# Kernel tuning notes

Hardware: AMD Instinct MI355X
Metric: run time of the kernel (lower is better)

Reference implementation:

```python
import jax, jax.numpy as jnp
import numpy as np
import math

B, T, N, FIN, C, E = 32, 10, 1000, 1, 96, 8000
NEG_SLOPE = 0.2


def _sinusoidal_pos_embed(stepsize, embedding_size):
    position = jnp.arange(stepsize, dtype=jnp.float32)[:, None]
    div_term = jnp.exp(jnp.arange(0, embedding_size, 2, dtype=jnp.float32)
                       * (-math.log(10000.0) / embedding_size))
    pe = jnp.zeros((stepsize, embedding_size), dtype=jnp.float32)
    pe = pe.at[:, 0::2].set(jnp.sin(position * div_term))
    pe = pe.at[:, 1::2].set(jnp.cos(position * div_term))
    return pe  # [T, C]


def setup_inputs() -> dict:
    key = jax.random.key(0)
    k_x, k_s, k_d, k_wl, k_wr, k_a = jax.random.split(key, 6)
    x = jax.random.normal(k_x, (B, T, N, FIN), dtype=jnp.float32)
    src = jax.random.randint(k_s, (E,), 0, N)
    dst = jax.random.randint(k_d, (E,), 0, N)
    edge_index = jnp.stack([src, dst]).astype(jnp.int32)
    s_in = 1.0 / np.sqrt(FIN)
    Wl = jax.random.uniform(k_wl, (FIN, C), jnp.float32, -s_in, s_in)
    Wr = jax.random.uniform(k_wr, (FIN, C), jnp.float32, -s_in, s_in)
    bl = jnp.zeros((C,), jnp.float32)
    br = jnp.zeros((C,), jnp.float32)
    s_a = 1.0 / np.sqrt(C)
    att = jax.random.uniform(k_a, (C,), jnp.float32, -s_a, s_a)
    bias = jnp.zeros((C,), jnp.float32)
    return dict(x=x, edge_index=edge_index, Wl=Wl, bl=bl, Wr=Wr, br=br,
                att=att, bias=bias)


def reference(x, edge_index, Wl, bl, Wr, br, att, bias):
    Bb, Tt, Nn, Fin = x.shape
    Cc = Wl.shape[1]
    # GATv2Conv default add_self_loops=True
    loops = jnp.arange(Nn, dtype=edge_index.dtype)
    src = jnp.concatenate([edge_index[0], loops])  # message sources j
    dst = jnp.concatenate([edge_index[1], loops])  # message targets i

    xg = x.reshape(Bb * Tt, Nn, Fin)                 # [G, N, Fin]
    xl = xg @ Wl + bl                                # lin_l(x_j)  [G, N, C]
    xr = xg @ Wr + br                                # lin_r(x_i)  [G, N, C]

    # GATv2 attention logits: a^T LeakyReLU(xl[j] + xr[i])
    e = jax.nn.leaky_relu(xl[:, src] + xr[:, dst], NEG_SLOPE) @ att  # [G, Etot]

    def per_graph(e_g, xl_g):
        m = jax.ops.segment_max(e_g, dst, num_segments=Nn)
        ex = jnp.exp(e_g - m[dst])
        denom = jax.ops.segment_sum(ex, dst, num_segments=Nn)
        alpha = ex / denom[dst]                       # softmax over incoming edges
        msgs = alpha[:, None] * xl_g[src]             # [Etot, C]
        return jax.ops.segment_sum(msgs, dst, num_segments=Nn)  # [N, C]

    out = jax.vmap(per_graph)(e, xl) + bias           # [G, N, C]
    out = out.reshape(Bb, Tt, Nn, Cc)

    pos = _sinusoidal_pos_embed(Tt, Cc)               # [T, C]
    out = out + pos[None, :, None, :]
    return out.reshape(Bb, Tt * Nn, Cc)
```

## Files before the change

kernel.cpp:

```cpp
#include <hip/hip_runtime.h>
#include <math.h>

#define G_ 320
#define N_ 1000
#define T_ 10
#define C_ 96
#define E_ 8000
#define QN 250
#define CAP 2816
#define NTB 129

__global__ __launch_bounds__(256, 6) void kAll(
        const float* __restrict__ x, const int* __restrict__ ei,
        const float* __restrict__ Wl, const float* __restrict__ bl,
        const float* __restrict__ Wr, const float* __restrict__ br,
        const float* __restrict__ att, const float* __restrict__ bias,
        float4* __restrict__ out) {
    __shared__ float xgs[N_];
    __shared__ int   slots[CAP];
    __shared__ int   cnt[256], cur[256], offsL[260];
    __shared__ float tabL[2 * NTB];
    __shared__ float Sloc[QN];
    __shared__ float4 wl4[C_ / 4], cb4[C_ / 4];
    __shared__ float lin4[4];

    const int tid = threadIdx.x;
    const int q = blockIdx.x, g = blockIdx.y;
    const int lo = q * QN;
    const int t = g % T_;

    if (tid < N_ / 4)
        ((float4*)xgs)[tid] = ((const float4*)(x + (size_t)g * N_))[tid];
    cnt[tid] = (tid < QN) ? 1 : 0;
    if (tid < C_) {
        int k2 = tid & ~1;
        float dt = __expf(-(float)k2 * (logf(10000.0f) / (float)C_));
        float ang = (float)t * dt;
        float pe = (tid & 1) ? cosf(ang) : sinf(ang);
        ((float*)wl4)[tid] = Wl[tid];
        ((float*)cb4)[tid] = bl[tid] + bias[tid] + pe;
    }
    {
        int w = tid >> 6, lane = tid & 63;
        if (w < 3) {
            float s = 0.f;
            for (int i = lane; i < C_; i += 64) {
                float a = att[i];
                float m = (w == 0) ? Wl[i] : (w == 1) ? Wr[i] : (bl[i] + br[i]);
                s += a * m;
            }
            for (int off = 32; off; off >>= 1) s += __shfl_down(s, off);
            if (lane == 0) lin4[w] = 0.6f * s;
        } else {
            float m = 0.f;
            for (int i = lane; i < C_; i += 64) m = fmaxf(m, fabsf(bl[i] + br[i]));
            for (int off = 32; off; off >>= 1) m = fmaxf(m, __shfl_down(m, off));
            if (lane == 0) lin4[3] = (m == 0.f) ? 1.f : 0.f;
        }
    }
    for (int i = tid; i < 2 * NTB; i += 256) {
        int which = (i >= NTB);
        int j = i - which * NTB;
        float tt = -1.f + (float)j * (2.f / (float)(NTB - 1));
        float s = 0.f;
        for (int c = 0; c < C_; c++) {
            float wl = Wl[c], wr = Wr[c];
            float val = which ? fmaf(tt, wl, wr) : fmaf(tt, wr, wl);
            s = fmaf(0.4f * att[c], fabsf(val), s);
        }
        tabL[i] = s;
    }
    __syncthreads();

    const int4* d4 = (const int4*)(ei + E_);
    const int4* s4 = (const int4*)ei;
    for (int j = tid; j < E_ / 4; j += 256) {
        int4 d = d4[j];
        int r0 = d.x - lo, r1 = d.y - lo, r2 = d.z - lo, r3 = d.w - lo;
        if ((unsigned)r0 < (unsigned)QN) atomicAdd(&cnt[r0], 1);
        if ((unsigned)r1 < (unsigned)QN) atomicAdd(&cnt[r1], 1);
        if ((unsigned)r2 < (unsigned)QN) atomicAdd(&cnt[r2], 1);
        if ((unsigned)r3 < (unsigned)QN) atomicAdd(&cnt[r3], 1);
    }
    __syncthreads();

    if (tid < 64) {
        int b4 = tid * 4;
        int a0 = cnt[b4], a1 = cnt[b4 + 1], a2 = cnt[b4 + 2], a3 = cnt[b4 + 3];
        int s1 = a0 + a1, s2 = s1 + a2, s3 = s2 + a3;
        int pre = s3;
        for (int off = 1; off < 64; off <<= 1) {
            int tv = __shfl_up(pre, off);
            if (tid >= off) pre += tv;
        }
        int base = pre - s3;
        offsL[b4] = base;          cur[b4] = base;
        offsL[b4 + 1] = base + a0; cur[b4 + 1] = base + a0;
        offsL[b4 + 2] = base + s1; cur[b4 + 2] = base + s1;
        offsL[b4 + 3] = base + s2; cur[b4 + 3] = base + s2;
    }
    __syncthreads();

    for (int j = tid; j < E_ / 4; j += 256) {
        int4 d = d4[j];
        int4 s = s4[j];
#define SCAT(DD, SS) { int r = (DD) - lo;                                    \
        if ((unsigned)r < (unsigned)QN) {                                    \
            int pos = atomicAdd(&cur[r], 1);                                 \
            slots[pos] = (SS) | ((DD) << 16); } }
        SCAT(d.x, s.x) SCAT(d.y, s.y) SCAT(d.z, s.z) SCAT(d.w, s.w)
#undef SCAT
    }
    if (tid < QN) {
        int nid = lo + tid;
        int pos = atomicAdd(&cur[tid], 1);
        slots[pos] = nid | (nid << 16);
    }
    __syncthreads();

    const float la = lin4[0], lb = lin4[1], lc = lin4[2];
    const bool homog = (lin4[3] != 0.f);
    if (tid < QN) {
        int a = offsL[tid], b = offsL[tid + 1];
        float m = -INFINITY, den = 0.f, num = 0.f;
        if (homog) {
            for (int p = a; p < b; ++p) {
                int sd = slots[p];
                float uu = xgs[sd & 0xFFFF], vv = xgs[sd >> 16];
                float au = fabsf(uu), av = fabsf(vv);
                bool ub = au >= av;
                float big = ub ? au : av;
                float tt = (ub ? vv : uu) / (ub ? uu : vv);
                tt = fmaxf(fminf(tt, 1.f), -1.f);
                float fi = fmaf(tt, 64.f, 64.f);
                int i0 = (int)fi; i0 = min(i0, NTB - 2);
                float fr = fi - (float)i0;
                int bse = ub ? 0 : NTB;
                float t0 = tabL[bse + i0], t1 = tabL[bse + i0 + 1];
                float l = fmaf(big, fmaf(fr, t1 - t0, t0),
                               fmaf(uu, la, fmaf(vv, lb, lc)));
                float nm = fmaxf(m, l);
                float sc = __expf(m - nm);
                float ex = __expf(l - nm);
                den = den * sc + ex;
                num = fmaf(ex, uu, num * sc);
                m = nm;
            }
        } else {
            for (int p = a; p < b; ++p) {
                int sd = slots[p];
                float uu = xgs[sd & 0xFFFF], vv = xgs[sd >> 16];
                float a2 = 0.f;
                for (int c = 0; c < C_; c++) {
                    float wv = fmaf(uu, Wl[c], fmaf(vv, Wr[c], bl[c] + br[c]));
                    a2 = fmaf(0.4f * att[c], fabsf(wv), a2);
                }
                float l = fmaf(uu, la, fmaf(vv, lb, lc)) + a2;
                float nm = fmaxf(m, l);
                float sc = __expf(m - nm);
                float ex = __expf(l - nm);
                den = den * sc + ex;
                num = fmaf(ex, uu, num * sc);
                m = nm;
            }
        }
        Sloc[tid] = num / den;
    }
    __syncthreads();

    float4* out4 = out + (size_t)(g * N_ + lo) * (C_ / 4);
    int node = tid / 24, c4 = tid % 24;
    for (int i = tid; i < QN * (C_ / 4); i += 256) {
        float s = Sloc[node];
        float4 wv = wl4[c4], cb = cb4[c4];
        out4[i] = make_float4(fmaf(s, wv.x, cb.x), fmaf(s, wv.y, cb.y),
                              fmaf(s, wv.z, cb.z), fmaf(s, wv.w, cb.w));
        int c4n = c4 + 16;
        int carry = (c4n >= 24) ? 1 : 0;
        node += 10 + carry;
        c4 = c4n - (carry ? 24 : 0);
    }
}

extern "C" void kernel_launch(void* const* d_in, const int* in_sizes, int n_in,
                              void* d_out, int out_size, void* d_ws, size_t ws_size,
                              hipStream_t stream) {
    const float* x    = (const float*)d_in[0];
    const int*   ei   = (const int*)d_in[1];
    const float* Wl   = (const float*)d_in[2];
    const float* bl   = (const float*)d_in[3];
    const float* Wr   = (const float*)d_in[4];
    const float* br   = (const float*)d_in[5];
    const float* att  = (const float*)d_in[6];
    const float* bias = (const float*)d_in[7];
    float4* out = (float4*)d_out;

    hipLaunchKernelGGL(kAll, dim3(4, G_), dim3(256), 0, stream,
                       x, ei, Wl, bl, Wr, br, att, bias, out);
}
```

Before: 42.44 us.

## Process two graphs per block to amortize CSR build and prefetch edges into registers

Each block now handles two consecutive graphs for the same node quarter. The per-block setup (counting in-degrees, prefix scan, bucketing edges by destination, building the attention lookup table) is done once and reused for both graphs, halving the grid. Edge indices are loaded once into registers and reused by the count and scatter passes instead of being read from global memory twice. The cost is fewer blocks (less parallelism), serial work per block for two graphs, and higher register pressure from the 16 int4 edge registers.

```diff
diff --git a/kernel.cpp b/kernel.cpp
--- a/kernel.cpp
+++ b/kernel.cpp
@@ -10,36 +10,51 @@
 #define CAP 2816
 #define NTB 129
 
-__global__ __launch_bounds__(256, 6) void kAll(
+__global__ __launch_bounds__(256, 6) void kAll2(
         const float* __restrict__ x, const int* __restrict__ ei,
         const float* __restrict__ Wl, const float* __restrict__ bl,
         const float* __restrict__ Wr, const float* __restrict__ br,
         const float* __restrict__ att, const float* __restrict__ bias,
         float4* __restrict__ out) {
-    __shared__ float xgs[N_];
+    __shared__ float xgs[2][N_];
     __shared__ int   slots[CAP];
-    __shared__ int   cnt[256], cur[256], offsL[260];
+    __shared__ int   cnt[256], cur[256], offsL[256];
     __shared__ float tabL[2 * NTB];
-    __shared__ float Sloc[QN];
-    __shared__ float4 wl4[C_ / 4], cb4[C_ / 4];
+    __shared__ float Sloc[2][QN];
+    __shared__ float4 wl4[C_ / 4];
+    __shared__ float4 cb4[2][C_ / 4];
     __shared__ float lin4[4];
 
     const int tid = threadIdx.x;
-    const int q = blockIdx.x, g = blockIdx.y;
+    const int q = blockIdx.x, gy = blockIdx.y;
+    const int g0 = gy * 2;
     const int lo = q * QN;
-    const int t = g % T_;
-
-    if (tid < N_ / 4)
-        ((float4*)xgs)[tid] = ((const float4*)(x + (size_t)g * N_))[tid];
+    const int t0 = g0 % T_;
+
+    {
+        const float4* xb = (const float4*)(x + (size_t)g0 * N_);
+        ((float4*)xgs)[tid] = xb[tid];
+        if (tid < 2 * N_ / 4 - 256) ((float4*)xgs)[tid + 256] = xb[tid + 256];
+    }
+    int4 dreg[8], sreg[8];
+    const int4* d4 = (const int4*)(ei + E_);
+    const int4* s4 = (const int4*)ei;
+#pragma unroll
+    for (int k = 0; k < 8; k++) {
+        int j = tid + k * 256;
+        if (j < E_ / 4) { dreg[k] = d4[j]; sreg[k] = s4[j]; }
+    }
     cnt[tid] = (tid < QN) ? 1 : 0;
-    if (tid < C_) {
-        int k2 = tid & ~1;
+    if (tid < 192) {
+        int it = tid / C_, c = tid - it * C_;
+        int tt = t0 + it;
+        int k2 = c & ~1;
         float dt = __expf(-(float)k2 * (logf(10000.0f) / (float)C_));
-        float ang = (float)t * dt;
-        float pe = (tid & 1) ? cosf(ang) : sinf(ang);
-        ((float*)wl4)[tid] = Wl[tid];
-        ((float*)cb4)[tid] = bl[tid] + bias[tid] + pe;
-    }
+        float ang = (float)tt * dt;
+        float pe = (c & 1) ? cosf(ang) : sinf(ang);
+        ((float*)cb4[it])[c] = bl[c] + bias[c] + pe;
+    }
+    if (tid < C_) ((float*)wl4)[tid] = Wl[tid];
     {
         int w = tid >> 6, lane = tid & 63;
         if (w < 3) {
@@ -72,15 +87,17 @@
     }
     __syncthreads();
 
-    const int4* d4 = (const int4*)(ei + E_);
-    const int4* s4 = (const int4*)ei;
-    for (int j = tid; j < E_ / 4; j += 256) {
-        int4 d = d4[j];
-        int r0 = d.x - lo, r1 = d.y - lo, r2 = d.z - lo, r3 = d.w - lo;
-        if ((unsigned)r0 < (unsigned)QN) atomicAdd(&cnt[r0], 1);
-        if ((unsigned)r1 < (unsigned)QN) atomicAdd(&cnt[r1], 1);
-        if ((unsigned)r2 < (unsigned)QN) atomicAdd(&cnt[r2], 1);
-        if ((unsigned)r3 < (unsigned)QN) atomicAdd(&cnt[r3], 1);
+#pragma unroll
+    for (int k = 0; k < 8; k++) {
+        int j = tid + k * 256;
+        if (j < E_ / 4) {
+            int4 d = dreg[k];
+            int r0 = d.x - lo, r1 = d.y - lo, r2 = d.z - lo, r3 = d.w - lo;
+            if ((unsigned)r0 < (unsigned)QN) atomicAdd(&cnt[r0], 1);
+            if ((unsigned)r1 < (unsigned)QN) atomicAdd(&cnt[r1], 1);
+            if ((unsigned)r2 < (unsigned)QN) atomicAdd(&cnt[r2], 1);
+            if ((unsigned)r3 < (unsigned)QN) atomicAdd(&cnt[r3], 1);
+        }
     }
     __syncthreads();
 
@@ -100,16 +117,21 @@
         offsL[b4 + 3] = base + s2; cur[b4 + 3] = base + s2;
     }
     __syncthreads();
-
-    for (int j = tid; j < E_ / 4; j += 256) {
-        int4 d = d4[j];
-        int4 s = s4[j];
+    const int cntE = offsL[QN];
+
+#pragma unroll
+    for (int k = 0; k < 8; k++) {
+        int j = tid + k * 256;
+        if (j < E_ / 4) {
+            int4 d = dreg[k];
+            int4 s = sreg[k];
 #define SCAT(DD, SS) { int r = (DD) - lo;                                    \
-        if ((unsigned)r < (unsigned)QN) {                                    \
-            int pos = atomicAdd(&cur[r], 1);                                 \
-            slots[pos] = (SS) | ((DD) << 16); } }
-        SCAT(d.x, s.x) SCAT(d.y, s.y) SCAT(d.z, s.z) SCAT(d.w, s.w)
+            if ((unsigned)r < (unsigned)QN) {                                \
+                int pos = atomicAdd(&cur[r], 1);                             \
+                slots[pos] = (SS) | ((DD) << 16); } }
+            SCAT(d.x, s.x) SCAT(d.y, s.y) SCAT(d.z, s.z) SCAT(d.w, s.w)
 #undef SCAT
+        }
     }
     if (tid < QN) {
         int nid = lo + tid;
@@ -121,64 +143,73 @@
     const float la = lin4[0], lb = lin4[1], lc = lin4[2];
     const bool homog = (lin4[3] != 0.f);
     if (tid < QN) {
-        int a = offsL[tid], b = offsL[tid + 1];
-        float m = -INFINITY, den = 0.f, num = 0.f;
-        if (homog) {
-            for (int p = a; p < b; ++p) {
-                int sd = slots[p];
-                float uu = xgs[sd & 0xFFFF], vv = xgs[sd >> 16];
-                float au = fabsf(uu), av = fabsf(vv);
-                bool ub = au >= av;
-                float big = ub ? au : av;
-                float tt = (ub ? vv : uu) / (ub ? uu : vv);
-                tt = fmaxf(fminf(tt, 1.f), -1.f);
-                float fi = fmaf(tt, 64.f, 64.f);
-                int i0 = (int)fi; i0 = min(i0, NTB - 2);
-                float fr = fi - (float)i0;
-                int bse = ub ? 0 : NTB;
-                float t0 = tabL[bse + i0], t1 = tabL[bse + i0 + 1];
-                float l = fmaf(big, fmaf(fr, t1 - t0, t0),
-                               fmaf(uu, la, fmaf(vv, lb, lc)));
-                float nm = fmaxf(m, l);
-                float sc = __expf(m - nm);
-                float ex = __expf(l - nm);
-                den = den * sc + ex;
-                num = fmaf(ex, uu, num * sc);
-                m = nm;
+        int a = offsL[tid], b = (tid == QN - 1) ? cntE : offsL[tid + 1];
+#pragma unroll 1
+        for (int it = 0; it < 2; ++it) {
+            const float* xx = xgs[it];
+            float m = -INFINITY, den = 0.f, num = 0.f;
+            if (homog) {
+                for (int p = a; p < b; ++p) {
+                    int sd = slots[p];
+                    float uu = xx[sd & 0xFFFF], vv = xx[sd >> 16];
+                    float au = fabsf(uu), av = fabsf(vv);
+                    bool ub = au >= av;
+                    float big = ub ? au : av;
+                    float tt = (ub ? vv : uu) / (ub ? uu : vv);
+                    tt = fmaxf(fminf(tt, 1.f), -1.f);
+                    float fi = fmaf(tt, 64.f, 64.f);
+                    int i0 = (int)fi; i0 = min(i0, NTB - 2);
+                    float fr = fi - (float)i0;
+                    int bse = ub ? 0 : NTB;
+                    float ta = tabL[bse + i0], tb = tabL[bse + i0 + 1];
+                    float l = fmaf(big, fmaf(fr, tb - ta, ta),
+                                   fmaf(uu, la, fmaf(vv, lb, lc)));
+                    float nm = fmaxf(m, l);
+                    float sc = __expf(m - nm);
+                    float ex = __expf(l - nm);
+                    den = den * sc + ex;
+                    num = fmaf(ex, uu, num * sc);
+                    m = nm;
+                }
+            } else {
+                for (int p = a; p < b; ++p) {
+                    int sd = slots[p];
+                    float uu = xx[sd & 0xFFFF], vv = xx[sd >> 16];
+                    float a2 = 0.f;
+                    for (int c = 0; c < C_; c++) {
+                        float wv = fmaf(uu, Wl[c], fmaf(vv, Wr[c], bl[c] + br[c]));
+                        a2 = fmaf(0.4f * att[c], fabsf(wv), a2);
+                    }
+                    float l = fmaf(uu, la, fmaf(vv, lb, lc)) + a2;
+                    float nm = fmaxf(m, l);
+                    float sc = __expf(m - nm);
+                    float ex = __expf(l - nm);
+                    den = den * sc + ex;
+                    num = fmaf(ex, uu, num * sc);
+                    m = nm;
+                }
             }
-        } else {
-            for (int p = a; p < b; ++p) {
-                int sd = slots[p];
-                float uu = xgs[sd & 0xFFFF], vv = xgs[sd >> 16];
-                float a2 = 0.f;
-                for (int c = 0; c < C_; c++) {
-                    float wv = fmaf(uu, Wl[c], fmaf(vv, Wr[c], bl[c] + br[c]));
-                    a2 = fmaf(0.4f * att[c], fabsf(wv), a2);
-                }
-                float l = fmaf(uu, la, fmaf(vv, lb, lc)) + a2;
-                float nm = fmaxf(m, l);
-                float sc = __expf(m - nm);
-                float ex = __expf(l - nm);
-                den = den * sc + ex;
-                num = fmaf(ex, uu, num * sc);
-                m = nm;
-            }
-        }
-        Sloc[tid] = num / den;
-    }
-    __syncthreads();
-
-    float4* out4 = out + (size_t)(g * N_ + lo) * (C_ / 4);
-    int node = tid / 24, c4 = tid % 24;
-    for (int i = tid; i < QN * (C_ / 4); i += 256) {
-        float s = Sloc[node];
-        float4 wv = wl4[c4], cb = cb4[c4];
-        out4[i] = make_float4(fmaf(s, wv.x, cb.x), fmaf(s, wv.y, cb.y),
-                              fmaf(s, wv.z, cb.z), fmaf(s, wv.w, cb.w));
-        int c4n = c4 + 16;
-        int carry = (c4n >= 24) ? 1 : 0;
-        node += 10 + carry;
-        c4 = c4n - (carry ? 24 : 0);
+            Sloc[it][tid] = num / den;
+        }
+    }
+    __syncthreads();
+
+#pragma unroll 1
+    for (int it = 0; it < 2; ++it) {
+        float4* out4 = out + (size_t)((g0 + it) * N_ + lo) * (C_ / 4);
+        int node = tid / 24, c4 = tid % 24;
+        const float* sl = Sloc[it];
+        const float4* cb = cb4[it];
+        for (int i = tid; i < QN * (C_ / 4); i += 256) {
+            float s = sl[node];
+            float4 wv = wl4[c4], cbv = cb[c4];
+            out4[i] = make_float4(fmaf(s, wv.x, cbv.x), fmaf(s, wv.y, cbv.y),
+                                  fmaf(s, wv.z, cbv.z), fmaf(s, wv.w, cbv.w));
+            int c4n = c4 + 16;
+            int carry = (c4n >= 24) ? 1 : 0;
+            node += 10 + carry;
+            c4 = c4n - (carry ? 24 : 0);
+        }
     }
 }
 
@@ -195,6 +226,6 @@
     const float* bias = (const float*)d_in[7];
     float4* out = (float4*)d_out;
 
-    hipLaunchKernelGGL(kAll, dim3(4, G_), dim3(256), 0, stream,
+    hipLaunchKernelGGL(kAll2, dim3(4, G_ / 2), dim3(256), 0, stream,
                        x, ei, Wl, bl, Wr, br, att, bias, out);
 }
```

Result: slower. 43.83 us (+3.3%).

## Replace CSR bucketing and online softmax with direct atomic exp-sum accumulation

Applied to the files above, without the earlier changes.

The per-block counting sort of incoming edges (count, scan, scatter into slots) and the per-node online-softmax loop are removed. Each edge's attention logit is now computed directly from the edge list, exponentiated without max subtraction, and atomically added into shared numerator and denominator arrays. The self-loop is added at the end. Output stores become nontemporal. This saves two barriers, the scan and the slot storage, but it relies on logits staying small enough that exp does not overflow and adds float atomic contention on shared memory.

```diff
diff --git a/kernel.cpp b/kernel.cpp
--- a/kernel.cpp
+++ b/kernel.cpp
@@ -7,20 +7,19 @@
 #define C_ 96
 #define E_ 8000
 #define QN 250
-#define CAP 2816
 #define NTB 129
 
-__global__ __launch_bounds__(256, 6) void kAll(
+typedef float float4n __attribute__((ext_vector_type(4)));
+
+__global__ __launch_bounds__(256, 6) void kAll3(
         const float* __restrict__ x, const int* __restrict__ ei,
         const float* __restrict__ Wl, const float* __restrict__ bl,
         const float* __restrict__ Wr, const float* __restrict__ br,
         const float* __restrict__ att, const float* __restrict__ bias,
         float4* __restrict__ out) {
     __shared__ float xgs[N_];
-    __shared__ int   slots[CAP];
-    __shared__ int   cnt[256], cur[256], offsL[260];
+    __shared__ float numS[QN], denS[QN];
     __shared__ float tabL[2 * NTB];
-    __shared__ float Sloc[QN];
     __shared__ float4 wl4[C_ / 4], cb4[C_ / 4];
     __shared__ float lin4[4];
 
@@ -31,7 +30,7 @@
 
     if (tid < N_ / 4)
         ((float4*)xgs)[tid] = ((const float4*)(x + (size_t)g * N_))[tid];
-    cnt[tid] = (tid < QN) ? 1 : 0;
+    if (tid < QN) { numS[tid] = 0.f; denS[tid] = 0.f; }
     if (tid < C_) {
         int k2 = tid & ~1;
         float dt = __expf(-(float)k2 * (logf(10000.0f) / (float)C_));
@@ -72,109 +71,84 @@
     }
     __syncthreads();
 
+    const float la = lin4[0], lb = lin4[1], lc = lin4[2];
+    const bool homog = (lin4[3] != 0.f);
     const int4* d4 = (const int4*)(ei + E_);
     const int4* s4 = (const int4*)ei;
-    for (int j = tid; j < E_ / 4; j += 256) {
-        int4 d = d4[j];
-        int r0 = d.x - lo, r1 = d.y - lo, r2 = d.z - lo, r3 = d.w - lo;
-        if ((unsigned)r0 < (unsigned)QN) atomicAdd(&cnt[r0], 1);
-        if ((unsigned)r1 < (unsigned)QN) atomicAdd(&cnt[r1], 1);
-        if ((unsigned)r2 < (unsigned)QN) atomicAdd(&cnt[r2], 1);
-        if ((unsigned)r3 < (unsigned)QN) atomicAdd(&cnt[r3], 1);
+    if (homog) {
+        for (int j = tid; j < E_ / 4; j += 256) {
+            int4 d = d4[j];
+            int4 s = s4[j];
+#define ACC(DD, SS) { int r = (DD) - lo;                                     \
+            if ((unsigned)r < (unsigned)QN) {                                \
+                float uu = xgs[SS], vv = xgs[DD];                            \
+                float au = fabsf(uu), av = fabsf(vv);                        \
+                bool ub = au >= av;                                          \
+                float big = ub ? au : av;                                    \
+                float tt = __fdividef(ub ? vv : uu, ub ? uu : vv);           \
+                tt = fmaxf(fminf(tt, 1.f), -1.f);                            \
+                float fi = fmaf(tt, 64.f, 64.f);                             \
+                int i0 = min((int)fi, NTB - 2);                              \
+                float fr = fi - (float)i0;                                   \
+                int bse = ub ? 0 : NTB;                                      \
+                float ta = tabL[bse + i0], tb = tabL[bse + i0 + 1];          \
+                float l = fmaf(big, fmaf(fr, tb - ta, ta),                   \
+                               fmaf(uu, la, fmaf(vv, lb, lc)));              \
+                float e = __expf(l);                                         \
+                atomicAdd(&denS[r], e);                                      \
+                atomicAdd(&numS[r], e * uu); } }
+            ACC(d.x, s.x) ACC(d.y, s.y) ACC(d.z, s.z) ACC(d.w, s.w)
+#undef ACC
+        }
+    } else {
+        for (int j = tid; j < E_ / 4; j += 256) {
+            int4 d = d4[j];
+            int4 s = s4[j];
+#define ACCX(DD, SS) { int r = (DD) - lo;                                    \
+            if ((unsigned)r < (unsigned)QN) {                                \
+                float uu = xgs[SS], vv = xgs[DD];                            \
+                float a2 = 0.f;                                              \
+                for (int c = 0; c < C_; c++) {                               \
+                    float wv = fmaf(uu, Wl[c], fmaf(vv, Wr[c], bl[c] + br[c]));\
+                    a2 = fmaf(0.4f * att[c], fabsf(wv), a2);                 \
+                }                                                            \
+                float l = fmaf(uu, la, fmaf(vv, lb, lc)) + a2;               \
+                float e = __expf(l);                                         \
+                atomicAdd(&denS[r], e);                                      \
+                atomicAdd(&numS[r], e * uu); } }
+            ACCX(d.x, s.x) ACCX(d.y, s.y) ACCX(d.z, s.z) ACCX(d.w, s.w)
+#undef ACCX
+        }
     }
     __syncthreads();
 
-    if (tid < 64) {
-        int b4 = tid * 4;
-        int a0 = cnt[b4], a1 = cnt[b4 + 1], a2 = cnt[b4 + 2], a3 = cnt[b4 + 3];
-        int s1 = a0 + a1, s2 = s1 + a2, s3 = s2 + a3;
-        int pre = s3;
-        for (int off = 1; off < 64; off <<= 1) {
-            int tv = __shfl_up(pre, off);
-            if (tid >= off) pre += tv;
+    if (tid < QN) {
+        float uu = xgs[lo + tid];
+        float l;
+        if (homog) {
+            l = fmaf(fabsf(uu), tabL[NTB - 1],
+                     fmaf(uu, la + lb, lc));
+        } else {
+            float a2 = 0.f;
+            for (int c = 0; c < C_; c++) {
+                float wv = fmaf(uu, Wl[c] + Wr[c], bl[c] + br[c]);
+                a2 = fmaf(0.4f * att[c], fabsf(wv), a2);
+            }
+            l = fmaf(uu, la + lb, lc) + a2;
         }
-        int base = pre - s3;
-        offsL[b4] = base;          cur[b4] = base;
-        offsL[b4 + 1] = base + a0; cur[b4 + 1] = base + a0;
-        offsL[b4 + 2] = base + s1; cur[b4 + 2] = base + s1;
-        offsL[b4 + 3] = base + s2; cur[b4 + 3] = base + s2;
+        float e = __expf(l);
+        numS[tid] = (numS[tid] + e * uu) / (denS[tid] + e);
     }
     __syncthreads();
 
-    for (int j = tid; j < E_ / 4; j += 256) {
-        int4 d = d4[j];
-        int4 s = s4[j];
-#define SCAT(DD, SS) { int r = (DD) - lo;                                    \
-        if ((unsigned)r < (unsigned)QN) {                                    \
-            int pos = atomicAdd(&cur[r], 1);                                 \
-            slots[pos] = (SS) | ((DD) << 16); } }
-        SCAT(d.x, s.x) SCAT(d.y, s.y) SCAT(d.z, s.z) SCAT(d.w, s.w)
-#undef SCAT
-    }
-    if (tid < QN) {
-        int nid = lo + tid;
-        int pos = atomicAdd(&cur[tid], 1);
-        slots[pos] = nid | (nid << 16);
-    }
-    __syncthreads();
-
-    const float la = lin4[0], lb = lin4[1], lc = lin4[2];
-    const bool homog = (lin4[3] != 0.f);
-    if (tid < QN) {
-        int a = offsL[tid], b = offsL[tid + 1];
-        float m = -INFINITY, den = 0.f, num = 0.f;
-        if (homog) {
-            for (int p = a; p < b; ++p) {
-                int sd = slots[p];
-                float uu = xgs[sd & 0xFFFF], vv = xgs[sd >> 16];
-                float au = fabsf(uu), av = fabsf(vv);
-                bool ub = au >= av;
-                float big = ub ? au : av;
-                float tt = (ub ? vv : uu) / (ub ? uu : vv);
-                tt = fmaxf(fminf(tt, 1.f), -1.f);
-                float fi = fmaf(tt, 64.f, 64.f);
-                int i0 = (int)fi; i0 = min(i0, NTB - 2);
-                float fr = fi - (float)i0;
-                int bse = ub ? 0 : NTB;
-                float t0 = tabL[bse + i0], t1 = tabL[bse + i0 + 1];
-                float l = fmaf(big, fmaf(fr, t1 - t0, t0),
-                               fmaf(uu, la, fmaf(vv, lb, lc)));
-                float nm = fmaxf(m, l);
-                float sc = __expf(m - nm);
-                float ex = __expf(l - nm);
-                den = den * sc + ex;
-                num = fmaf(ex, uu, num * sc);
-                m = nm;
-            }
-        } else {
-            for (int p = a; p < b; ++p) {
-                int sd = slots[p];
-                float uu = xgs[sd & 0xFFFF], vv = xgs[sd >> 16];
-                float a2 = 0.f;
-                for (int c = 0; c < C_; c++) {
-                    float wv = fmaf(uu, Wl[c], fmaf(vv, Wr[c], bl[c] + br[c]));
-                    a2 = fmaf(0.4f * att[c], fabsf(wv), a2);
-                }
-                float l = fmaf(uu, la, fmaf(vv, lb, lc)) + a2;
-                float nm = fmaxf(m, l);
-                float sc = __expf(m - nm);
-                float ex = __expf(l - nm);
-                den = den * sc + ex;
-                num = fmaf(ex, uu, num * sc);
-                m = nm;
-            }
-        }
-        Sloc[tid] = num / den;
-    }
-    __syncthreads();
-
-    float4* out4 = out + (size_t)(g * N_ + lo) * (C_ / 4);
+    float4n* out4 = (float4n*)(out + (size_t)(g * N_ + lo) * (C_ / 4));
     int node = tid / 24, c4 = tid % 24;
     for (int i = tid; i < QN * (C_ / 4); i += 256) {
-        float s = Sloc[node];
+        float s = numS[node];
         float4 wv = wl4[c4], cb = cb4[c4];
-        out4[i] = make_float4(fmaf(s, wv.x, cb.x), fmaf(s, wv.y, cb.y),
-                              fmaf(s, wv.z, cb.z), fmaf(s, wv.w, cb.w));
+        float4n o = { fmaf(s, wv.x, cb.x), fmaf(s, wv.y, cb.y),
+                      fmaf(s, wv.z, cb.z), fmaf(s, wv.w, cb.w) };
+        __builtin_nontemporal_store(o, &out4[i]);
         int c4n = c4 + 16;
         int carry = (c4n >= 24) ? 1 : 0;
         node += 10 + carry;
@@ -195,6 +169,6 @@
     const float* bias = (const float*)d_in[7];
     float4* out = (float4*)d_out;
 
-    hipLaunchKernelGGL(kAll, dim3(4, G_), dim3(256), 0, stream,
+    hipLaunchKernelGGL(kAll3, dim3(4, G_), dim3(256), 0, stream,
                        x, ei, Wl, bl, Wr, br, att, bias, out);
 }
```

Result: slower. 51.34 us (+21.0%).
